# Kernel tuning notes

Hardware: AMD Instinct MI355X
Metric: run time of the kernel (lower is better)

The kernel has to match this reference:

```python
import jax, jax.numpy as jnp
import numpy as np

# Static rendering config (from init_kwargs)
H, W, D = 128, 128, 64          # image height, width, depth samples
PIXEL = 1.0                      # pixel size
EXTENT_Z = 128.0
DZ = EXTENT_Z / D                # z spacing = 2.0
HIDDEN = 64                      # field MLP hidden dim
MD, MH, MW = 128, 128, 128       # mask volume shape


def _axis(n, s):
    # arange(n) - n/2 + 0.5, scaled: centered grid axis (center_grid_origin=True)
    return (jnp.arange(n, dtype=jnp.float32) - n / 2 + 0.5) * s


def make_base_grid():
    # cartesian_prod(px, py, pz, [1]) reshaped to [H, W, D, 4] == meshgrid 'ij'
    px, py, pz = _axis(H, PIXEL), _axis(W, PIXEL), _axis(D, DZ)
    gx, gy, gz = jnp.meshgrid(px, py, pz, indexing='ij')
    return jnp.stack([gx, gy, gz, jnp.ones_like(gx)], axis=-1)  # [H,W,D,4]


def trilinear_zeros(vol, xyz):
    """torch F.grid_sample 3D, bilinear, padding_mode='zeros', align_corners=True.
    vol: [Dm,Hm,Wm]; xyz: [N,3] normalized coords in [-1,1], x indexes W, y->H, z->D."""
    Dm, Hm, Wm = vol.shape
    x = (xyz[:, 0] + 1.0) * 0.5 * (Wm - 1)
    y = (xyz[:, 1] + 1.0) * 0.5 * (Hm - 1)
    z = (xyz[:, 2] + 1.0) * 0.5 * (Dm - 1)
    x0, y0, z0 = jnp.floor(x), jnp.floor(y), jnp.floor(z)
    fx, fy, fz = x - x0, y - y0, z - z0
    out = jnp.zeros_like(x)
    for dz_ in (0, 1):
        for dy_ in (0, 1):
            for dx_ in (0, 1):
                xi, yi, zi = x0 + dx_, y0 + dy_, z0 + dz_
                w = ((fx if dx_ else 1.0 - fx)
                     * (fy if dy_ else 1.0 - fy)
                     * (fz if dz_ else 1.0 - fz))
                valid = ((xi >= 0) & (xi <= Wm - 1) & (yi >= 0) & (yi <= Hm - 1)
                         & (zi >= 0) & (zi <= Dm - 1))
                v = vol[jnp.clip(zi, 0, Dm - 1).astype(jnp.int32),
                        jnp.clip(yi, 0, Hm - 1).astype(jnp.int32),
                        jnp.clip(xi, 0, Wm - 1).astype(jnp.int32)]
                out = out + w * jnp.where(valid, v, 0.0)
    return out


def setup_inputs() -> dict:
    key = jax.random.key(0)
    k1, k2, k3, k4 = jax.random.split(key, 4)
    # rigid rotation (last row [0,0,0,1]) so homogeneous w stays 1
    th, ph = 0.3, 0.5
    c, s = np.cos(th), np.sin(th)
    c2, s2 = np.cos(ph), np.sin(ph)
    Rz = np.array([[c, -s, 0, 0], [s, c, 0, 0], [0, 0, 1, 0], [0, 0, 0, 1]], np.float32)
    Rx = np.array([[1, 0, 0, 0], [0, c2, -s2, 0], [0, s2, c2, 0], [0, 0, 0, 1]], np.float32)
    T = jnp.asarray(Rz @ Rx)[None]  # [1,4,4]
    mask_vol = (jax.random.uniform(k1, (MD, MH, MW)) > 0.4).astype(jnp.float32)
    W1 = jax.random.normal(k2, (3, HIDDEN), jnp.float32) * 0.5
    b1 = jax.random.normal(k3, (HIDDEN,), jnp.float32) * 0.1
    W2 = jax.random.normal(k4, (HIDDEN, 1), jnp.float32) * 0.2
    b2 = jnp.zeros((1,), jnp.float32)
    return {"transform_matrix": T, "mask_vol": mask_vol,
            "W1": W1, "b1": b1, "W2": W2, "b2": b2}


def reference(transform_matrix, mask_vol, W1, b1, W2, b2):
    base = make_base_grid().reshape(-1, 4)           # [N,4], N = H*W*D
    T = transform_matrix[0]                          # [4,4]
    q = base @ T.T                                   # transformed homogeneous points [N,4]
    # setup_masked_buffers: normalize to [-1,1] by max |coord| of the base grid
    max_abs = jnp.max(jnp.abs(base[:, :3]))
    norm_xyz = q[:, :3] / max_abs
    m_interp = trilinear_zeros(mask_vol, norm_xyz)   # trilinear mask sample [N]
    mask = (m_interp != 0).astype(jnp.float32)       # .to(torch.bool) cast
    # forward: homogeneous divide, field eval (masked points only; here mask-weighted)
    q3 = q[:, :3] / q[:, 3:4]                        # [N,3]
    h = jax.nn.relu(q3 @ W1 + b1)                    # [N,HIDDEN]
    pot = (h @ W2 + b2)[:, 0]                        # [N]
    # segment_sum_csr over contiguous depth bins == sum over z axis per pixel
    img = jnp.sum((pot * mask).reshape(H, W, D), axis=-1) * DZ  # [H,W]
    return img[None]                                 # [1,H,W] (batch 1)
```

## Files before the change

### kernel.cpp

```cpp
#include <hip/hip_runtime.h>


#define NH 128
#define NW 128
#define ND 64
#define HID 64

__global__ __launch_bounds__(256) void dmp_kernel(
    const float* __restrict__ T,
    const float* __restrict__ vol,
    const float* __restrict__ W1,
    const float* __restrict__ b1,
    const float* __restrict__ W2,
    const float* __restrict__ b2,
    float* __restrict__ out)
{
    const int t   = blockIdx.x * 256 + threadIdx.x;
    const int d   = t & 63;
    const int pix = t >> 6;
    const int h   = pix >> 7;
    const int w   = pix & 127;

    const float bx = (float)h - 63.5f;
    const float by = (float)w - 63.5f;
    const float bz = ((float)d - 31.5f) * 2.0f;

    const float q0 = T[0]  * bx + T[1]  * by + T[2]  * bz + T[3];
    const float q1 = T[4]  * bx + T[5]  * by + T[6]  * bz + T[7];
    const float q2 = T[8]  * bx + T[9]  * by + T[10] * bz + T[11];
    const float qw = T[12] * bx + T[13] * by + T[14] * bz + T[15];

    const float inv_max = 1.0f / 63.5f;
    const float nx = q0 * inv_max;
    const float ny = q1 * inv_max;
    const float nz = q2 * inv_max;

    const float xf = (nx + 1.0f) * 0.5f * 127.0f;
    const float yf = (ny + 1.0f) * 0.5f * 127.0f;
    const float zf = (nz + 1.0f) * 0.5f * 127.0f;
    const float x0 = floorf(xf), y0 = floorf(yf), z0 = floorf(zf);
    const float fx = xf - x0, fy = yf - y0, fz = zf - z0;

    float m = 0.0f;
    #pragma unroll
    for (int dz_ = 0; dz_ < 2; ++dz_) {
        #pragma unroll
        for (int dy_ = 0; dy_ < 2; ++dy_) {
            #pragma unroll
            for (int dx_ = 0; dx_ < 2; ++dx_) {
                const float xi = x0 + (float)dx_;
                const float yi = y0 + (float)dy_;
                const float zi = z0 + (float)dz_;
                const float wgt = (dx_ ? fx : 1.0f - fx)
                                * (dy_ ? fy : 1.0f - fy)
                                * (dz_ ? fz : 1.0f - fz);
                const bool valid = (xi >= 0.0f) && (xi <= 127.0f)
                                && (yi >= 0.0f) && (yi <= 127.0f)
                                && (zi >= 0.0f) && (zi <= 127.0f);
                const int xc = min(max((int)xi, 0), 127);
                const int yc = min(max((int)yi, 0), 127);
                const int zc = min(max((int)zi, 0), 127);
                const float v = vol[(zc * 128 + yc) * 128 + xc];
                m += wgt * (valid ? v : 0.0f);
            }
        }
    }
    const float mask = (m != 0.0f) ? 1.0f : 0.0f;

    const float invw = 1.0f / qw;
    const float p0 = q0 * invw, p1 = q1 * invw, p2 = q2 * invw;
    float pot = b2[0];
    #pragma unroll 8
    for (int j = 0; j < HID; ++j) {
        float hj = p0 * W1[j] + p1 * W1[64 + j] + p2 * W1[128 + j] + b1[j];
        hj = fmaxf(hj, 0.0f);
        pot += hj * W2[j];
    }

    float val = pot * mask;
    #pragma unroll
    for (int off = 32; off > 0; off >>= 1)
        val += __shfl_down(val, off);

    if (d == 0)
        out[pix] = val * 2.0f;
}

extern "C" void kernel_launch(void* const* d_in, const int* in_sizes, int n_in,
                              void* d_out, int out_size, void* d_ws, size_t ws_size,
                              hipStream_t stream) {
    const float* T   = (const float*)d_in[0];
    const float* vol = (const float*)d_in[1];
    const float* W1  = (const float*)d_in[2];
    const float* b1  = (const float*)d_in[3];
    const float* W2  = (const float*)d_in[4];
    const float* b2  = (const float*)d_in[5];
    float* out = (float*)d_out;

    const int n_points = NH * NW * ND;
    dmp_kernel<<<n_points / 256, 256, 0, stream>>>(T, vol, W1, b1, W2, b2, out);
}
```

Measured before the change: 87.18 us.

## Pack mask volume into bitmask and skip wavefronts with no mask contribution

Adds a pre-pass kernel that packs the 128^3 float mask volume into a 1-bit-per-voxel bitmap using wavefront ballots, so the trilinear gathers read a 256KB array instead of 8MB. The main kernel now skips the 8 gathers when no lane in the wavefront touches the volume, and skips the 64-wide MLP when no lane has a nonzero mask. The mask test now checks the sum of corner weights for nonzero voxels rather than the weighted voxel values, which matches for non-negative masks but could differ if values cancel. It also adds a second kernel launch and assumes the workspace is large enough.

New measurement: 86.77 us. About the same (-0.5%).

```diff
diff --git a/kernel.cpp b/kernel.cpp
--- a/kernel.cpp
+++ b/kernel.cpp
@@ -6,9 +6,20 @@
 #define ND 64
 #define HID 64
 
+__global__ __launch_bounds__(256) void pack_kernel(
+    const float* __restrict__ vol,
+    unsigned long long* __restrict__ bits)
+{
+    const int t = blockIdx.x * 256 + threadIdx.x;
+    const float v = vol[t];
+    const unsigned long long b = __ballot(v != 0.0f);
+    if ((threadIdx.x & 63) == 0)
+        bits[t >> 6] = b;
+}
+
 __global__ __launch_bounds__(256) void dmp_kernel(
     const float* __restrict__ T,
-    const float* __restrict__ vol,
+    const unsigned int* __restrict__ bw,
     const float* __restrict__ W1,
     const float* __restrict__ b1,
     const float* __restrict__ W2,
@@ -41,43 +52,53 @@
     const float x0 = floorf(xf), y0 = floorf(yf), z0 = floorf(zf);
     const float fx = xf - x0, fy = yf - y0, fz = zf - z0;
 
+    const bool lane_touch = (xf >= -1.0f) && (x0 <= 127.0f)
+                         && (yf >= -1.0f) && (y0 <= 127.0f)
+                         && (zf >= -1.0f) && (z0 <= 127.0f);
+
     float m = 0.0f;
-    #pragma unroll
-    for (int dz_ = 0; dz_ < 2; ++dz_) {
+    if (__any(lane_touch)) {
         #pragma unroll
-        for (int dy_ = 0; dy_ < 2; ++dy_) {
+        for (int dz_ = 0; dz_ < 2; ++dz_) {
             #pragma unroll
-            for (int dx_ = 0; dx_ < 2; ++dx_) {
-                const float xi = x0 + (float)dx_;
-                const float yi = y0 + (float)dy_;
-                const float zi = z0 + (float)dz_;
-                const float wgt = (dx_ ? fx : 1.0f - fx)
-                                * (dy_ ? fy : 1.0f - fy)
-                                * (dz_ ? fz : 1.0f - fz);
-                const bool valid = (xi >= 0.0f) && (xi <= 127.0f)
-                                && (yi >= 0.0f) && (yi <= 127.0f)
-                                && (zi >= 0.0f) && (zi <= 127.0f);
-                const int xc = min(max((int)xi, 0), 127);
-                const int yc = min(max((int)yi, 0), 127);
-                const int zc = min(max((int)zi, 0), 127);
-                const float v = vol[(zc * 128 + yc) * 128 + xc];
-                m += wgt * (valid ? v : 0.0f);
+            for (int dy_ = 0; dy_ < 2; ++dy_) {
+                #pragma unroll
+                for (int dx_ = 0; dx_ < 2; ++dx_) {
+                    const float xi = x0 + (float)dx_;
+                    const float yi = y0 + (float)dy_;
+                    const float zi = z0 + (float)dz_;
+                    const float wgt = (dx_ ? fx : 1.0f - fx)
+                                    * (dy_ ? fy : 1.0f - fy)
+                                    * (dz_ ? fz : 1.0f - fz);
+                    const bool valid = (xi >= 0.0f) && (xi <= 127.0f)
+                                    && (yi >= 0.0f) && (yi <= 127.0f)
+                                    && (zi >= 0.0f) && (zi <= 127.0f);
+                    const int xc = min(max((int)xi, 0), 127);
+                    const int yc = min(max((int)yi, 0), 127);
+                    const int zc = min(max((int)zi, 0), 127);
+                    const unsigned int word = bw[((zc << 7) + yc) * 4 + (xc >> 5)];
+                    const bool bit = (word >> (xc & 31)) & 1u;
+                    m += (valid && bit) ? wgt : 0.0f;
+                }
             }
         }
     }
     const float mask = (m != 0.0f) ? 1.0f : 0.0f;
 
-    const float invw = 1.0f / qw;
-    const float p0 = q0 * invw, p1 = q1 * invw, p2 = q2 * invw;
-    float pot = b2[0];
-    #pragma unroll 8
-    for (int j = 0; j < HID; ++j) {
-        float hj = p0 * W1[j] + p1 * W1[64 + j] + p2 * W1[128 + j] + b1[j];
-        hj = fmaxf(hj, 0.0f);
-        pot += hj * W2[j];
+    float val = 0.0f;
+    if (__any(mask != 0.0f)) {
+        const float invw = 1.0f / qw;
+        const float p0 = q0 * invw, p1 = q1 * invw, p2 = q2 * invw;
+        float pot = b2[0];
+        #pragma unroll 8
+        for (int j = 0; j < HID; ++j) {
+            float hj = p0 * W1[j] + p1 * W1[64 + j] + p2 * W1[128 + j] + b1[j];
+            hj = fmaxf(hj, 0.0f);
+            pot += hj * W2[j];
+        }
+        val = pot * mask;
     }
 
-    float val = pot * mask;
     #pragma unroll
     for (int off = 32; off > 0; off >>= 1)
         val += __shfl_down(val, off);
@@ -97,6 +118,11 @@
     const float* b2  = (const float*)d_in[5];
     float* out = (float*)d_out;
 
+    unsigned long long* bits = (unsigned long long*)d_ws;
+
+    pack_kernel<<<8192, 256, 0, stream>>>(vol, bits);
+
     const int n_points = NH * NW * ND;
-    dmp_kernel<<<n_points / 256, 256, 0, stream>>>(T, vol, W1, b1, W2, b2, out);
+    dmp_kernel<<<n_points / 256, 256, 0, stream>>>(
+        T, (const unsigned int*)bits, W1, b1, W2, b2, out);
 }
```

## Pack mask volume into bitmask and skip MLP for fully masked wavefronts

Applied to the files above, without the earlier changes.

Adds a pre-pass that packs the mask volume into one bit per voxel using wavefront ballots. The main kernel tests whether a point's mask is nonzero with a few 16-byte bitmask loads instead of eight float gathers. It skips the 64-wide MLP for wavefronts with no active points, and vectorises the weight loads to float2. The cost is an extra kernel launch and pass over the 8 MB volume. The mask test now relies on nonzero weight and nonzero voxel implying a nonzero sum, which assumes non-negative mask values.

After: 88.90 us. No clear change (+2.0%).

```diff
diff --git a/kernel.cpp b/kernel.cpp
--- a/kernel.cpp
+++ b/kernel.cpp
@@ -5,10 +5,25 @@
 #define NW 128
 #define ND 64
 #define HID 64
+#define BITS_PAD 4096
+
+typedef unsigned long long u64;
+typedef unsigned int u32;
+
+__global__ __launch_bounds__(256) void pack_kernel(
+    const float* __restrict__ vol,
+    u64* __restrict__ bits)
+{
+    const int t = blockIdx.x * 256 + threadIdx.x;
+    const float v = vol[t];
+    const u64 b = __ballot(v != 0.0f);
+    if ((threadIdx.x & 63) == 0)
+        bits[t >> 6] = b;
+}
 
 __global__ __launch_bounds__(256) void dmp_kernel(
     const float* __restrict__ T,
-    const float* __restrict__ vol,
+    const char* __restrict__ ws,
     const float* __restrict__ W1,
     const float* __restrict__ b1,
     const float* __restrict__ W2,
@@ -31,56 +46,77 @@
     const float qw = T[12] * bx + T[13] * by + T[14] * bz + T[15];
 
     const float inv_max = 1.0f / 63.5f;
-    const float nx = q0 * inv_max;
-    const float ny = q1 * inv_max;
-    const float nz = q2 * inv_max;
+    const float xf = (q0 * inv_max + 1.0f) * 0.5f * 127.0f;
+    const float yf = (q1 * inv_max + 1.0f) * 0.5f * 127.0f;
+    const float zf = (q2 * inv_max + 1.0f) * 0.5f * 127.0f;
+    const float x0f = floorf(xf), y0f = floorf(yf), z0f = floorf(zf);
+    const float fx = xf - x0f, fy = yf - y0f, fz = zf - z0f;
 
-    const float xf = (nx + 1.0f) * 0.5f * 127.0f;
-    const float yf = (ny + 1.0f) * 0.5f * 127.0f;
-    const float zf = (nz + 1.0f) * 0.5f * 127.0f;
-    const float x0 = floorf(xf), y0 = floorf(yf), z0 = floorf(zf);
-    const float fx = xf - x0, fy = yf - y0, fz = zf - z0;
+    const bool uz0 = (z0f >= 0.0f)  && (z0f <= 127.0f) && ((1.0f - fz) != 0.0f);
+    const bool uz1 = (z0f >= -1.0f) && (z0f <= 126.0f) && (fz != 0.0f);
+    const bool uy0 = (y0f >= 0.0f)  && (y0f <= 127.0f) && ((1.0f - fy) != 0.0f);
+    const bool uy1 = (y0f >= -1.0f) && (y0f <= 126.0f) && (fy != 0.0f);
+    const bool ux0 = (x0f >= 0.0f)  && (x0f <= 127.0f) && ((1.0f - fx) != 0.0f);
+    const bool ux1 = (x0f >= -1.0f) && (x0f <= 126.0f) && (fx != 0.0f);
 
-    float m = 0.0f;
-    #pragma unroll
-    for (int dz_ = 0; dz_ < 2; ++dz_) {
-        #pragma unroll
-        for (int dy_ = 0; dy_ < 2; ++dy_) {
-            #pragma unroll
-            for (int dx_ = 0; dx_ < 2; ++dx_) {
-                const float xi = x0 + (float)dx_;
-                const float yi = y0 + (float)dy_;
-                const float zi = z0 + (float)dz_;
-                const float wgt = (dx_ ? fx : 1.0f - fx)
-                                * (dy_ ? fy : 1.0f - fy)
-                                * (dz_ ? fz : 1.0f - fz);
-                const bool valid = (xi >= 0.0f) && (xi <= 127.0f)
-                                && (yi >= 0.0f) && (yi <= 127.0f)
-                                && (zi >= 0.0f) && (zi <= 127.0f);
-                const int xc = min(max((int)xi, 0), 127);
-                const int yc = min(max((int)yi, 0), 127);
-                const int zc = min(max((int)zi, 0), 127);
-                const float v = vol[(zc * 128 + yc) * 128 + xc];
-                m += wgt * (valid ? v : 0.0f);
-            }
-        }
-    }
-    const float mask = (m != 0.0f) ? 1.0f : 0.0f;
+    const bool lane_active = (uz0 | uz1) && (uy0 | uy1) && (ux0 | ux1);
 
-    const float invw = 1.0f / qw;
-    const float p0 = q0 * invw, p1 = q1 * invw, p2 = q2 * invw;
-    float pot = b2[0];
-    #pragma unroll 8
-    for (int j = 0; j < HID; ++j) {
-        float hj = p0 * W1[j] + p1 * W1[64 + j] + p2 * W1[128 + j] + b1[j];
-        hj = fmaxf(hj, 0.0f);
-        pot += hj * W2[j];
+    bool mask = false;
+    if (__any(lane_active)) {
+        const int iz = min(max((int)z0f, -1), 127);
+        const int iy = min(max((int)y0f, -1), 127);
+        const int off = BITS_PAD + (iz << 11) + (iy << 4);
+
+        const uint4 r00 = *(const uint4*)(ws + off);
+        const uint4 r01 = *(const uint4*)(ws + off + 16);
+        const uint4 r10 = *(const uint4*)(ws + off + 2048);
+        const uint4 r11 = *(const uint4*)(ws + off + 2064);
+
+        u64 lo = 0, hi = 0;
+        if (uz0 & uy0) { lo |= ((u64)r00.y << 32) | r00.x; hi |= ((u64)r00.w << 32) | r00.z; }
+        if (uz0 & uy1) { lo |= ((u64)r01.y << 32) | r01.x; hi |= ((u64)r01.w << 32) | r01.z; }
+        if (uz1 & uy0) { lo |= ((u64)r10.y << 32) | r10.x; hi |= ((u64)r10.w << 32) | r10.z; }
+        if (uz1 & uy1) { lo |= ((u64)r11.y << 32) | r11.x; hi |= ((u64)r11.w << 32) | r11.z; }
+
+        const int ix0 = (int)x0f;
+        const int c0 = min(max(ix0, 0), 127);
+        const int c1 = min(max(ix0 + 1, 0), 127);
+        const u64 s0 = (c0 & 64) ? hi : lo;
+        const u64 s1 = (c1 & 64) ? hi : lo;
+        const bool b0 = (s0 >> (c0 & 63)) & 1ull;
+        const bool b1 = (s1 >> (c1 & 63)) & 1ull;
+
+        mask = (b0 & ux0) | (b1 & ux1);
     }
 
-    float val = pot * mask;
+    float val = 0.0f;
+    if (__any(mask)) {
+        const float invw = 1.0f / qw;
+        const float p0 = q0 * invw, p1 = q1 * invw, p2 = q2 * invw;
+        const float2* W1a = (const float2*)W1;
+        const float2* W1b = (const float2*)(W1 + 64);
+        const float2* W1c = (const float2*)(W1 + 128);
+        const float2* B1  = (const float2*)b1;
+        const float2* W2v = (const float2*)W2;
+        float sx = 0.0f, sy = 0.0f;
+        #pragma unroll 8
+        for (int j = 0; j < HID / 2; ++j) {
+            const float2 wa = W1a[j], wb = W1b[j], wc = W1c[j];
+            const float2 bb = B1[j],  w2 = W2v[j];
+            float hx = fmaf(p0, wa.x, fmaf(p1, wb.x, fmaf(p2, wc.x, bb.x)));
+            float hy = fmaf(p0, wa.y, fmaf(p1, wb.y, fmaf(p2, wc.y, bb.y)));
+            hx = fmaxf(hx, 0.0f);
+            hy = fmaxf(hy, 0.0f);
+            sx = fmaf(hx, w2.x, sx);
+            sy = fmaf(hy, w2.y, sy);
+        }
+        const float pot = sx + sy + b2[0];
+        val = mask ? pot : 0.0f;
+    }
+
     #pragma unroll
-    for (int off = 32; off > 0; off >>= 1)
-        val += __shfl_down(val, off);
+    for (int off2 = 32; off2 > 0; off2 >>= 1)
+        val += __shfl_down(val, off2);
 
     if (d == 0)
         out[pix] = val * 2.0f;
@@ -97,6 +133,11 @@
     const float* b2  = (const float*)d_in[5];
     float* out = (float*)d_out;
 
+    u64* bits = (u64*)((char*)d_ws + BITS_PAD);
+
+    pack_kernel<<<8192, 256, 0, stream>>>(vol, bits);
+
     const int n_points = NH * NW * ND;
-    dmp_kernel<<<n_points / 256, 256, 0, stream>>>(T, vol, W1, b1, W2, b2, out);
+    dmp_kernel<<<n_points / 256, 256, 0, stream>>>(
+        T, (const char*)d_ws, W1, b1, W2, b2, out);
 }
```
